# Kernel tuning notes

Measured on AMD Instinct MI355X. Metric: run time of the kernel, lower is better.

The kernel has to match this reference:

```python
import jax, jax.numpy as jnp
import numpy as np

B, S, H = 2, 2048, 1024
NH, HD = 16, 64  # num heads, head dim


def setup_inputs() -> dict:
    key = jax.random.key(0)
    ks = jax.random.split(key, 8)
    scale = 0.02
    return {
        "hidden_states": jax.random.normal(ks[0], (B, S, H), dtype=jnp.float32),
        "attention_mask": jnp.zeros((B, 1, 1, S), dtype=jnp.float32),
        "Wq": jax.random.normal(ks[1], (H, H), dtype=jnp.float32) * scale,
        "bq": jnp.zeros((H,), dtype=jnp.float32),
        "Wk": jax.random.normal(ks[2], (H, H), dtype=jnp.float32) * scale,
        "bk": jnp.zeros((H,), dtype=jnp.float32),
        "Wv": jax.random.normal(ks[3], (H, H), dtype=jnp.float32) * scale,
        "bv": jnp.zeros((H,), dtype=jnp.float32),
    }


def _split_heads(x):
    # [B,S,H] -> [B,NH,S,HD]
    b, s, _ = x.shape
    return x.reshape(b, s, NH, HD).transpose(0, 2, 1, 3)


def reference(hidden_states, attention_mask, Wq, bq, Wk, bk, Wv, bv):
    q = _split_heads(hidden_states @ Wq.T + bq)
    k = _split_heads(hidden_states @ Wk.T + bk)
    v = _split_heads(hidden_states @ Wv.T + bv)
    # scores: [B,NH,S,S]
    scores = jnp.einsum("bhqd,bhkd->bhqk", q, k) / jnp.sqrt(jnp.float32(HD))
    scores = scores + attention_mask
    att = jax.nn.softmax(scores, axis=-1)  # dropout is identity in eval
    ctx = jnp.einsum("bhqk,bhkd->bhqd", att, v)
    # [B,NH,S,HD] -> [B,S,H]
    return ctx.transpose(0, 2, 1, 3).reshape(hidden_states.shape[0], hidden_states.shape[1], NH * HD)
```

## Files before the change

### kernel.cpp

```cpp
#include <hip/hip_runtime.h>
#include <stdint.h>

#define BB 2
#define SS 2048
#define HH 1024
#define NH 16
#define HD 64

#define LOG2E 1.4426950408889634f
#define QSCALE (0.125f * LOG2E)

typedef short bfrag  __attribute__((ext_vector_type(8)));
typedef short bfrag4 __attribute__((ext_vector_type(4)));
typedef float f32x4  __attribute__((ext_vector_type(4)));

__device__ __forceinline__ short f2bf(float f) {
    union { float f; uint32_t u; } v; v.f = f;
    uint32_t r = (v.u + 0x7fffu + ((v.u >> 16) & 1u)) >> 16;
    return (short)r;
}

__device__ __forceinline__ uint32_t pack_bf16(float a, float b) {
#if __has_builtin(__builtin_amdgcn_cvt_pk_bf16_f32)
    auto t = __builtin_amdgcn_cvt_pk_bf16_f32(a, b);
    uint32_t u; __builtin_memcpy(&u, &t, 4);
    return u;
#else
    uint32_t ua = __float_as_uint(a) + 0x8000u;
    uint32_t ub = __float_as_uint(b) + 0x8000u;
    return __builtin_amdgcn_perm(ub, ua, 0x07060302u);
#endif
}

__global__ __launch_bounds__(256) void cvt_all(
    const float* __restrict__ X,  const float* __restrict__ Wq,
    const float* __restrict__ Wk, const float* __restrict__ Wv,
    const float* __restrict__ mask,
    short* __restrict__ Xb, short* __restrict__ Wcat,
    float* __restrict__ maskl)
{
    int i = blockIdx.x * 256 + threadIdx.x;
    if (i >= 1835008) {
        int off = i - 1835008;
        float4 f = ((const float4*)mask)[off];
        f.x *= LOG2E; f.y *= LOG2E; f.z *= LOG2E; f.w *= LOG2E;
        ((float4*)maskl)[off] = f;
        return;
    }
    const float* src; short* dst; int off;
    if (i < 1048576)      { src = X;  dst = Xb;                 off = i; }
    else if (i < 1310720) { src = Wq; dst = Wcat;               off = i - 1048576; }
    else if (i < 1572864) { src = Wk; dst = Wcat + 1048576;     off = i - 1310720; }
    else                  { src = Wv; dst = Wcat + 2097152;     off = i - 1572864; }
    float4 f = ((const float4*)src)[off];
    short4 s;
    s.x = f2bf(f.x); s.y = f2bf(f.y); s.z = f2bf(f.z); s.w = f2bf(f.w);
    ((short4*)dst)[off] = s;
}

__device__ __forceinline__ void gload_lds16(const void* g, void* lds) {
    __builtin_amdgcn_global_load_lds(
        (__attribute__((address_space(1))) void*)(uintptr_t)g,
        (__attribute__((address_space(3))) void*)(uintptr_t)lds,
        16, 0, 0);
}

__global__ __launch_bounds__(256, 3) void qkv_gemm(
    const short* __restrict__ X, const short* __restrict__ Wcat,
    const float* __restrict__ bq, const float* __restrict__ bk, const float* __restrict__ bv,
    short* __restrict__ Qo, short* __restrict__ Ko, short* __restrict__ Vo)
{
    __shared__ __align__(16) short smem[17408];

    const int tid  = threadIdx.x;
    const int wave = tid >> 6, lane = tid & 63;
    const int quad = lane >> 4, l15 = lane & 15;
    const int mTile = blockIdx.y * 128;
    const int nTile = blockIdx.x * 128;
    const int z = nTile >> 10;
    const int nLocT = nTile & 1023;
    const float* bias = (z == 0) ? bq : (z == 1) ? bk : bv;

    f32x4 acc[4][4];
#pragma unroll
    for (int i = 0; i < 4; ++i)
#pragma unroll
        for (int j = 0; j < 4; ++j) acc[i][j] = (f32x4)0.0f;

    const int srow  = lane >> 3;
    const int c_lin = lane & 7;
    const int mBase = (wave >> 1) * 64;
    const int nBase = (wave & 1) * 64;

    for (int k0 = 0; k0 < 1024; k0 += 64) {
        __syncthreads();
#pragma unroll
        for (int i = 0; i < 4; ++i) {
            int row = i * 32 + wave * 8 + srow;
            int cg  = c_lin ^ (row & 7);
            gload_lds16(X + (size_t)(mTile + row) * 1024 + k0 + cg * 8,
                        (char*)smem + i * 4096 + wave * 1024);
            gload_lds16(Wcat + (size_t)(nTile + row) * 1024 + k0 + cg * 8,
                        (char*)smem + 16384 + i * 4096 + wave * 1024);
        }
        __syncthreads();

#pragma unroll
        for (int kt = 0; kt < 2; ++kt) {
            bfrag af[4], bf[4];
#pragma unroll
            for (int t = 0; t < 4; ++t) {
                int arow = mBase + t * 16 + l15;
                int aslot = (kt * 4 + quad) ^ (arow & 7);
                af[t] = *(const bfrag*)((const char*)smem + arow * 128 + aslot * 16);
                int brow = nBase + t * 16 + l15;
                int bslot = (kt * 4 + quad) ^ (brow & 7);
                bf[t] = *(const bfrag*)((const char*)smem + 16384 + brow * 128 + bslot * 16);
            }
#pragma unroll
            for (int mt = 0; mt < 4; ++mt)
#pragma unroll
                for (int ct = 0; ct < 4; ++ct)
                    acc[mt][ct] = __builtin_amdgcn_mfma_f32_16x16x32_bf16(
                        af[mt], bf[ct], acc[mt][ct], 0, 0, 0);
        }
    }

    __syncthreads();
    const int b = mTile >> 11, sBase = mTile & 2047;

    if (z == 2) {
#pragma unroll
        for (int mt = 0; mt < 4; ++mt)
#pragma unroll
            for (int ct = 0; ct < 4; ++ct)
#pragma unroll
                for (int r = 0; r < 4; ++r) {
                    int nl = nBase + ct * 16 + l15;
                    int sl = mBase + mt * 16 + quad * 4 + r;
                    smem[nl * 136 + sl] = f2bf(acc[mt][ct][r] + bias[nLocT + nl]);
                }
        __syncthreads();
#pragma unroll
        for (int p = 0; p < 8; ++p) {
            int nl = p * 16 + (tid >> 4);
            int cg = tid & 15;
            int blk = cg >> 3;
            int c2  = cg & 7;
            int base = blk * 64 + (c2 >> 2) * 32 + (c2 & 3) * 4;
            int2 lo = *(const int2*)(smem + nl * 136 + base);
            int2 hi = *(const int2*)(smem + nl * 136 + base + 16);
            int4 v; v.x = lo.x; v.y = lo.y; v.z = hi.x; v.w = hi.y;
            int ng = nLocT + nl, hh = ng >> 6, d = ng & 63;
            *(int4*)(Vo + ((size_t)(b * 16 + hh) * 64 + d) * 2048 + sBase + cg * 8) = v;
        }
    } else {
        short* Out = (z == 0) ? Qo : Ko;
        float scale = (z == 0) ? QSCALE : 1.0f;
#pragma unroll
        for (int mt = 0; mt < 4; ++mt)
#pragma unroll
            for (int ct = 0; ct < 4; ++ct)
#pragma unroll
                for (int r = 0; r < 4; ++r) {
                    int ml = mBase + mt * 16 + quad * 4 + r;
                    int nl = nBase + ct * 16 + l15;
                    smem[ml * 136 + nl] = f2bf((acc[mt][ct][r] + bias[nLocT + nl]) * scale);
                }
        __syncthreads();
#pragma unroll
        for (int p = 0; p < 8; ++p) {
            int ml = p * 16 + (tid >> 4);
            int c  = tid & 15;
            bfrag v8 = *(const bfrag*)(smem + ml * 136 + c * 8);
            int s  = sBase + ml;
            int nl = nLocT + c * 8, hh = nl >> 6, d = nl & 63;
            *(bfrag*)(Out + (((size_t)(b * 16 + hh) << 11) + s) * 64 + d) = v8;
        }
    }
}

__global__ __launch_bounds__(256, 2) void attn_kernel(
    const short* __restrict__ Qb, const short* __restrict__ Kb, const short* __restrict__ Vb,
    const float* __restrict__ maskl, float* __restrict__ out)
{
    __shared__ __align__(16) char smem[32768];

    const int tid  = threadIdx.x;
    const int wave = tid >> 6, lane = tid & 63;
    const int quad = lane >> 4, l15 = lane & 15;

    const int id = blockIdx.x;
    const int slot = id >> 3;
    const int bh = ((id & 7) << 2) | (slot & 3);
    const int qt = slot >> 2;
    const int b  = bh >> 4, h = bh & 15;
    const int qBase = qt * 128 + wave * 32;

    int ksrc[2], vsrc[2];
#pragma unroll
    for (int i = 0; i < 2; ++i) {
        int ci = wave * 128 + i * 64 + lane;
        int r = ci >> 3, c = ci & 7;
        int cs = (c ^ (r & 7)) * 16;
        ksrc[i] = r * 128  + cs;
        vsrc[i] = r * 4096 + cs;
    }
    const char* kBase = (const char*)(Kb + (size_t)bh * SS * HD);
    const char* vBase = (const char*)(Vb + (size_t)bh * HD * SS);
    const char* mSrc  = (const char*)(maskl + b * SS) + quad * 16;

    const short* Qp = Qb + ((size_t)bh * SS + qBase) * HD;
    bfrag qf[2][2];
#pragma unroll
    for (int hf = 0; hf < 2; ++hf)
#pragma unroll
        for (int kt = 0; kt < 2; ++kt)
            qf[hf][kt] = *(const bfrag*)(Qp + (size_t)(hf * 16 + l15) * HD + kt * 32 + quad * 8);

    int kAddr[2];
#pragma unroll
    for (int kt = 0; kt < 2; ++kt)
        kAddr[kt] = l15 * 128 + (((kt * 4 + quad) ^ (l15 & 7)) * 16);
    int vAddr[2];
#pragma unroll
    for (int g = 0; g < 2; ++g)
        vAddr[g] = 8192 + l15 * 128 + (((g * 4 + quad) ^ (l15 & 7)) * 16);

    const f32x4 z4 = (f32x4)0.0f;
    const bfrag ones8 = {0x3F80, 0x3F80, 0x3F80, 0x3F80,
                         0x3F80, 0x3F80, 0x3F80, 0x3F80};

    f32x4 oacc[2][4], ol[2];
#pragma unroll
    for (int hf = 0; hf < 2; ++hf) {
        ol[hf] = z4;
#pragma unroll
        for (int dt = 0; dt < 4; ++dt) oacc[hf][dt] = z4;
    }

#pragma unroll
    for (int i = 0; i < 2; ++i) {
        gload_lds16(kBase + ksrc[i], smem + wave * 2048 + i * 1024);
        gload_lds16(vBase + vsrc[i], smem + 8192 + wave * 2048 + i * 1024);
    }

    auto astep = [&](int CUR, int NXT, int jn, int pref) {
        __syncthreads();
        if (pref) {
#pragma unroll
            for (int i = 0; i < 2; ++i) {
                gload_lds16(kBase + jn * 8192 + ksrc[i], smem + NXT + wave * 2048 + i * 1024);
                gload_lds16(vBase + jn * 128  + vsrc[i], smem + NXT + 8192 + wave * 2048 + i * 1024);
            }
        }

        f32x4 mvl[4];
#pragma unroll
        for (int ct = 0; ct < 4; ++ct)
            mvl[ct] = *(const f32x4*)(mSrc + ct * 64);
        mSrc += 256;

        f32x4 s0[4], s1[4];
#pragma unroll
        for (int ct = 0; ct < 4; ++ct) {
            bfrag kf0 = *(const bfrag*)(smem + CUR + kAddr[0] + ct * 2048);
            bfrag kf1 = *(const bfrag*)(smem + CUR + kAddr[1] + ct * 2048);
            s0[ct] = __builtin_amdgcn_mfma_f32_16x16x32_bf16(kf0, qf[0][0], mvl[ct], 0, 0, 0);
            s0[ct] = __builtin_amdgcn_mfma_f32_16x16x32_bf16(kf1, qf[0][1], s0[ct],  0, 0, 0);
            s1[ct] = __builtin_amdgcn_mfma_f32_16x16x32_bf16(kf0, qf[1][0], mvl[ct], 0, 0, 0);
            s1[ct] = __builtin_amdgcn_mfma_f32_16x16x32_bf16(kf1, qf[1][1], s1[ct],  0, 0, 0);
        }

        bfrag p0[2], p1[2];
#pragma unroll
        for (int g = 0; g < 2; ++g) {
            union { uint32_t u[4]; bfrag v; } cvt;
            cvt.u[0] = pack_bf16(__builtin_amdgcn_exp2f(s0[2*g][0]),   __builtin_amdgcn_exp2f(s0[2*g][1]));
            cvt.u[1] = pack_bf16(__builtin_amdgcn_exp2f(s0[2*g][2]),   __builtin_amdgcn_exp2f(s0[2*g][3]));
            cvt.u[2] = pack_bf16(__builtin_amdgcn_exp2f(s0[2*g+1][0]), __builtin_amdgcn_exp2f(s0[2*g+1][1]));
            cvt.u[3] = pack_bf16(__builtin_amdgcn_exp2f(s0[2*g+1][2]), __builtin_amdgcn_exp2f(s0[2*g+1][3]));
            p0[g] = cvt.v;
            cvt.u[0] = pack_bf16(__builtin_amdgcn_exp2f(s1[2*g][0]),   __builtin_amdgcn_exp2f(s1[2*g][1]));
            cvt.u[1] = pack_bf16(__builtin_amdgcn_exp2f(s1[2*g][2]),   __builtin_amdgcn_exp2f(s1[2*g][3]));
            cvt.u[2] = pack_bf16(__builtin_amdgcn_exp2f(s1[2*g+1][0]), __builtin_amdgcn_exp2f(s1[2*g+1][1]));
            cvt.u[3] = pack_bf16(__builtin_amdgcn_exp2f(s1[2*g+1][2]), __builtin_amdgcn_exp2f(s1[2*g+1][3]));
            p1[g] = cvt.v;
        }

#pragma unroll
        for (int dt = 0; dt < 4; ++dt) {
#pragma unroll
            for (int g = 0; g < 2; ++g) {
                bfrag v = *(const bfrag*)(smem + CUR + vAddr[g] + dt * 2048);
                oacc[0][dt] = __builtin_amdgcn_mfma_f32_16x16x32_bf16(p0[g], v, oacc[0][dt], 0, 0, 0);
                oacc[1][dt] = __builtin_amdgcn_mfma_f32_16x16x32_bf16(p1[g], v, oacc[1][dt], 0, 0, 0);
            }
        }
#pragma unroll
        for (int g = 0; g < 2; ++g) {
            ol[0] = __builtin_amdgcn_mfma_f32_16x16x32_bf16(p0[g], ones8, ol[0], 0, 0, 0);
            ol[1] = __builtin_amdgcn_mfma_f32_16x16x32_bf16(p1[g], ones8, ol[1], 0, 0, 0);
        }
    };

    for (int jj = 0; jj < 16; ++jj) {
        astep(0,     16384, 2 * jj + 1, 1);
        astep(16384, 0,     2 * jj + 2, jj < 15);
    }

#pragma unroll
    for (int hf = 0; hf < 2; ++hf) {
#pragma unroll
        for (int r = 0; r < 4; ++r) {
            float linv = 1.0f / ol[hf][r];
            int qrow = qBase + hf * 16 + quad * 4 + r;
#pragma unroll
            for (int dt = 0; dt < 4; ++dt)
                out[((size_t)(b * SS + qrow)) * HH + h * 64 + dt * 16 + l15] =
                    oacc[hf][dt][r] * linv;
        }
    }
}

extern "C" void kernel_launch(void* const* d_in, const int* in_sizes, int n_in,
                              void* d_out, int out_size, void* d_ws, size_t ws_size,
                              hipStream_t stream) {
    const float* hs   = (const float*)d_in[0];
    const float* mask = (const float*)d_in[1];
    const float* Wq   = (const float*)d_in[2];
    const float* bq   = (const float*)d_in[3];
    const float* Wk   = (const float*)d_in[4];
    const float* bk   = (const float*)d_in[5];
    const float* Wv   = (const float*)d_in[6];
    const float* bv   = (const float*)d_in[7];
    float* out = (float*)d_out;

    char* ws = (char*)d_ws;
    short* Xb    = (short*)(ws);
    short* Wcat  = (short*)(ws + (8ull  << 20));
    short* Qb    = (short*)(ws + (14ull << 20));
    short* Kb    = (short*)(ws + (22ull << 20));
    short* Vb    = (short*)(ws + (30ull << 20));
    float* maskl = (float*)(ws + (38ull << 20));

    cvt_all<<<7172, 256, 0, stream>>>(hs, Wq, Wk, Wv, mask, Xb, Wcat, maskl);

    qkv_gemm<<<dim3(24, 32), 256, 0, stream>>>(Xb, Wcat, bq, bk, bv, Qb, Kb, Vb);

    attn_kernel<<<512, 256, 0, stream>>>(Qb, Kb, Vb, maskl, out);
}
```

Baseline: 157.9 us.

## Split attention KV range in two halves with atomic accumulation and normalize pass

Splits each attention block's key/value range into two halves, doubling the grid to 1024 blocks, and raises launch bounds to 4 blocks per CU. Partial outputs are combined with float atomicAdd into a zeroed output, and per-half row sums go to a workspace array. A separate normalize kernel then divides by the summed row sums. It also adds s_setprio around the MFMA sections. The goal is more parallelism and occupancy, at the cost of a memset, atomic traffic, an extra kernel launch and another read and write of the output.

```diff
diff --git a/kernel.cpp b/kernel.cpp
--- a/kernel.cpp
+++ b/kernel.cpp
@@ -11,7 +11,6 @@
 #define QSCALE (0.125f * LOG2E)
 
 typedef short bfrag  __attribute__((ext_vector_type(8)));
-typedef short bfrag4 __attribute__((ext_vector_type(4)));
 typedef float f32x4  __attribute__((ext_vector_type(4)));
 
 __device__ __forceinline__ short f2bf(float f) {
@@ -180,9 +179,9 @@
     }
 }
 
-__global__ __launch_bounds__(256, 2) void attn_kernel(
+__global__ __launch_bounds__(256, 4) void attn_kernel(
     const short* __restrict__ Qb, const short* __restrict__ Kb, const short* __restrict__ Vb,
-    const float* __restrict__ maskl, float* __restrict__ out)
+    const float* __restrict__ maskl, float* __restrict__ out, float* __restrict__ lpart)
 {
     __shared__ __align__(16) char smem[32768];
 
@@ -193,9 +192,12 @@
     const int id = blockIdx.x;
     const int slot = id >> 3;
     const int bh = ((id & 7) << 2) | (slot & 3);
-    const int qt = slot >> 2;
+    const int r2 = slot >> 2;
+    const int qt = r2 & 15;
+    const int half = r2 >> 4;
     const int b  = bh >> 4, h = bh & 15;
     const int qBase = qt * 128 + wave * 32;
+    const int t0 = half * 16;
 
     int ksrc[2], vsrc[2];
 #pragma unroll
@@ -208,7 +210,7 @@
     }
     const char* kBase = (const char*)(Kb + (size_t)bh * SS * HD);
     const char* vBase = (const char*)(Vb + (size_t)bh * HD * SS);
-    const char* mSrc  = (const char*)(maskl + b * SS) + quad * 16;
+    const char* mSrc  = (const char*)(maskl + b * SS + half * 1024) + quad * 16;
 
     const short* Qp = Qb + ((size_t)bh * SS + qBase) * HD;
     bfrag qf[2][2];
@@ -241,8 +243,8 @@
 
 #pragma unroll
     for (int i = 0; i < 2; ++i) {
-        gload_lds16(kBase + ksrc[i], smem + wave * 2048 + i * 1024);
-        gload_lds16(vBase + vsrc[i], smem + 8192 + wave * 2048 + i * 1024);
+        gload_lds16(kBase + (size_t)t0 * 8192 + ksrc[i], smem + wave * 2048 + i * 1024);
+        gload_lds16(vBase + (size_t)t0 * 128  + vsrc[i], smem + 8192 + wave * 2048 + i * 1024);
     }
 
     auto astep = [&](int CUR, int NXT, int jn, int pref) {
@@ -250,8 +252,10 @@
         if (pref) {
 #pragma unroll
             for (int i = 0; i < 2; ++i) {
-                gload_lds16(kBase + jn * 8192 + ksrc[i], smem + NXT + wave * 2048 + i * 1024);
-                gload_lds16(vBase + jn * 128  + vsrc[i], smem + NXT + 8192 + wave * 2048 + i * 1024);
+                gload_lds16(kBase + (size_t)jn * 8192 + ksrc[i],
+                            smem + NXT + wave * 2048 + i * 1024);
+                gload_lds16(vBase + (size_t)jn * 128  + vsrc[i],
+                            smem + NXT + 8192 + wave * 2048 + i * 1024);
             }
         }
 
@@ -262,6 +266,7 @@
         mSrc += 256;
 
         f32x4 s0[4], s1[4];
+        __builtin_amdgcn_s_setprio(1);
 #pragma unroll
         for (int ct = 0; ct < 4; ++ct) {
             bfrag kf0 = *(const bfrag*)(smem + CUR + kAddr[0] + ct * 2048);
@@ -271,6 +276,7 @@
             s1[ct] = __builtin_amdgcn_mfma_f32_16x16x32_bf16(kf0, qf[1][0], mvl[ct], 0, 0, 0);
             s1[ct] = __builtin_amdgcn_mfma_f32_16x16x32_bf16(kf1, qf[1][1], s1[ct],  0, 0, 0);
         }
+        __builtin_amdgcn_s_setprio(0);
 
         bfrag p0[2], p1[2];
 #pragma unroll
@@ -288,6 +294,7 @@
             p1[g] = cvt.v;
         }
 
+        __builtin_amdgcn_s_setprio(1);
 #pragma unroll
         for (int dt = 0; dt < 4; ++dt) {
 #pragma unroll
@@ -302,25 +309,45 @@
             ol[0] = __builtin_amdgcn_mfma_f32_16x16x32_bf16(p0[g], ones8, ol[0], 0, 0, 0);
             ol[1] = __builtin_amdgcn_mfma_f32_16x16x32_bf16(p1[g], ones8, ol[1], 0, 0, 0);
         }
+        __builtin_amdgcn_s_setprio(0);
     };
 
-    for (int jj = 0; jj < 16; ++jj) {
-        astep(0,     16384, 2 * jj + 1, 1);
-        astep(16384, 0,     2 * jj + 2, jj < 15);
+    for (int jj = 0; jj < 8; ++jj) {
+        astep(0,     16384, t0 + 2 * jj + 1, 1);
+        astep(16384, 0,     t0 + 2 * jj + 2, jj < 7);
     }
 
 #pragma unroll
     for (int hf = 0; hf < 2; ++hf) {
 #pragma unroll
         for (int r = 0; r < 4; ++r) {
-            float linv = 1.0f / ol[hf][r];
             int qrow = qBase + hf * 16 + quad * 4 + r;
+            int row2 = (((bh << 11) + qrow) << 1) + half;
+            lpart[row2] = ol[hf][r];
 #pragma unroll
             for (int dt = 0; dt < 4; ++dt)
-                out[((size_t)(b * SS + qrow)) * HH + h * 64 + dt * 16 + l15] =
-                    oacc[hf][dt][r] * linv;
-        }
-    }
+                atomicAdd(&out[((size_t)(b * SS + qrow)) * HH + h * 64 + dt * 16 + l15],
+                          oacc[hf][dt][r]);
+        }
+    }
+}
+
+__global__ __launch_bounds__(256) void normalize_kernel(
+    const float* __restrict__ lpart, float* __restrict__ out)
+{
+    int id = blockIdx.x * 256 + threadIdx.x;
+    int f  = id << 2;
+    int bs = f >> 10;
+    int hd = f & 1023;
+    int h  = hd >> 6;
+    int b  = bs >> 11, s = bs & 2047;
+    int bh = b * 16 + h;
+    int base = (((bh << 11) + s) << 1);
+    float linv = 1.0f / (lpart[base] + lpart[base + 1]);
+    f32x4 v = ((const f32x4*)out)[id];
+#pragma unroll
+    for (int j = 0; j < 4; ++j) v[j] *= linv;
+    ((f32x4*)out)[id] = v;
 }
 
 extern "C" void kernel_launch(void* const* d_in, const int* in_sizes, int n_in,
@@ -337,16 +364,21 @@
     float* out = (float*)d_out;
 
     char* ws = (char*)d_ws;
-    short* Xb    = (short*)(ws);
-    short* Wcat  = (short*)(ws + (8ull  << 20));
-    short* Qb    = (short*)(ws + (14ull << 20));
-    short* Kb    = (short*)(ws + (22ull << 20));
-    short* Vb    = (short*)(ws + (30ull << 20));
-    float* maskl = (float*)(ws + (38ull << 20));
+    short* Qb    = (short*)(ws);
+    short* Kb    = (short*)(ws + (8ull  << 20));
+    short* Vb    = (short*)(ws + (16ull << 20));
+    float* maskl = (float*)(ws + (24ull << 20));
+    float* lpart = (float*)(ws + (24ull << 20) + 65536);
+    short* Xb    = (short*)(ws + (25ull << 20));
+    short* Wcat  = (short*)(ws + (33ull << 20));
+
+    hipMemsetAsync(out, 0, out_size, stream);
 
     cvt_all<<<7172, 256, 0, stream>>>(hs, Wq, Wk, Wv, mask, Xb, Wcat, maskl);
 
     qkv_gemm<<<dim3(24, 32), 256, 0, stream>>>(Xb, Wcat, bq, bk, bv, Qb, Kb, Vb);
 
-    attn_kernel<<<512, 256, 0, stream>>>(Qb, Kb, Vb, maskl, out);
-}
+    attn_kernel<<<1024, 256, 0, stream>>>(Qb, Kb, Vb, maskl, out, lpart);
+
+    normalize_kernel<<<4096, 256, 0, stream>>>(lpart, out);
+}
```

New measurement: 198.8 us. +25.9%, slower.
